# Kernel tuning notes

Hardware: AMD Instinct MI355X
Metric: run time of the kernel (lower is better)

The kernel has to match this reference:

```python
import jax, jax.numpy as jnp
import numpy as np

N, IN_DIM, OUT_DIM = 50000, 256, 64
K, DELTA_D = 8, 8            # k = out_dim // (ndim // init_k) = 64 // (64 // 8)
M = 1638400                  # edges
ROUTIT, TAU = 4, 1.0
EPS = 1e-12                  # F.normalize eps


def _l2norm(v, n, k, dd):
    # F.normalize over last dim of (n, k, dd) view, flattened back to (n, k*dd)
    v = v.reshape(n, k, dd)
    nrm = jnp.sqrt(jnp.sum(v * v, axis=2, keepdims=True))
    v = v / jnp.maximum(nrm, EPS)
    return v.reshape(n, k * dd)


def setup_inputs() -> dict:
    key = jax.random.key(0)
    k1, k2, k3, k4 = jax.random.split(key, 4)
    x = jax.random.normal(k1, (N, IN_DIM), dtype=jnp.float32)
    src_trg = jax.random.randint(k2, (2, M), 0, N, dtype=jnp.int64)
    std = 1.0 / np.sqrt(OUT_DIM)
    weight = jax.random.uniform(k3, (IN_DIM, OUT_DIM), dtype=jnp.float32, minval=-std, maxval=std)
    bias = jax.random.uniform(k4, (OUT_DIM,), dtype=jnp.float32, minval=-std, maxval=std)
    return {"x": x, "src_trg": src_trg, "weight": weight, "bias": bias}


def reference(x, src_trg, weight, bias):
    trg, src = src_trg[0], src_trg[1]
    n = x.shape[0]
    d = K * DELTA_D
    # DimReduceLayer + leaky_relu + per-capsule L2 normalize
    h = jax.nn.leaky_relu(x @ weight + bias)          # (n, d)
    h = _l2norm(h, n, K, DELTA_D)
    # RoutingLayer normalizes again (idempotent up to eps, kept for fidelity)
    h = _l2norm(h, n, K, DELTA_D)
    z = h[src].reshape(M, K, DELTA_D)                  # gather source capsules
    c = h
    for _ in range(ROUTIT):
        ct = c[trg].reshape(M, K, DELTA_D)             # gather target capsules
        p = jnp.sum(z * ct, axis=2)                    # (m, k) per-edge capsule scores
        p = jax.nn.softmax(p / TAU, axis=1)
        ws = (p[:, :, None] * z).reshape(M, d)         # weighted messages
        c = c.at[trg].add(ws)                          # scatter-add into targets
        c = _l2norm(c, n, K, DELTA_D)
    return c
```

## Files before the change

kernel.cpp:

```cpp
#include <hip/hip_runtime.h>
#include <math.h>
#include <stdint.h>

#define IN_DIM 256
#define OUT_D 64
#define ROUTIT 4
#define LCAP 48
#define NG 6
#define BSH 7
#define NBMAX 512
#define PEDGES 8192
#define LCCAP 6144

typedef float v2f __attribute__((ext_vector_type(2)));
__device__ __forceinline__ v2f pk_fma(v2f a, v2f b, v2f c) {
    return __builtin_elementwise_fma(a, b, c);
}

__device__ __forceinline__ float dpp_add_xor1(float x) {
    return x + __int_as_float(__builtin_amdgcn_mov_dpp(__float_as_int(x), 0xB1, 0xF, 0xF, true));
}
__device__ __forceinline__ float dpp_add_xor2(float x) {
    return x + __int_as_float(__builtin_amdgcn_mov_dpp(__float_as_int(x), 0x4E, 0xF, 0xF, true));
}
__device__ __forceinline__ float dpp_add_xor8(float x) {
    return x + __int_as_float(__builtin_amdgcn_mov_dpp(__float_as_int(x), 0x128, 0xF, 0xF, true));
}
__device__ __forceinline__ float swz_add_xor4(float x) {
    return x + __int_as_float(__builtin_amdgcn_ds_swizzle(__float_as_int(x), 0x101F));
}
__device__ __forceinline__ float swz_add_xor16(float x) {
    return x + __int_as_float(__builtin_amdgcn_ds_swizzle(__float_as_int(x), 0x401F));
}

__device__ __forceinline__ void load8p(v2f z[4], const float* p) {
    float4 a = *(const float4*)p;
    float4 b = *(const float4*)(p + 4);
    z[0] = (v2f){a.x, a.y}; z[1] = (v2f){a.z, a.w};
    z[2] = (v2f){b.x, b.y}; z[3] = (v2f){b.z, b.w};
}

__global__ __launch_bounds__(512, 2) void gemm_norm_kernel(
    const float* __restrict__ x, const float* __restrict__ w,
    const float* __restrict__ bias, float* __restrict__ h, int n)
{
    __shared__ float wlds[IN_DIM * OUT_D];
    {
        const float4* wsrc = (const float4*)w;
        float4* wdst = (float4*)wlds;
        #pragma unroll
        for (int i = 0; i < (IN_DIM * OUT_D / 4); i += 512)
            wdst[i + threadIdx.x] = wsrc[i + threadIdx.x];
    }
    __syncthreads();

    int lane = threadIdx.x & 63;
    int wv   = threadIdx.x >> 6;
    int c0   = wv * 8;
    int base = blockIdx.x * 256;

    const float* xr[4];
    int rows[4];
    #pragma unroll
    for (int r = 0; r < 4; ++r) {
        rows[r] = base + r * 64 + lane;
        int rc = rows[r] < n ? rows[r] : n - 1;
        xr[r] = x + (size_t)rc * IN_DIM;
    }

    v2f b2[4];
    #pragma unroll
    for (int j = 0; j < 4; ++j) b2[j] = (v2f){bias[c0 + 2*j], bias[c0 + 2*j + 1]};
    v2f acc[4][4];
    #pragma unroll
    for (int r = 0; r < 4; ++r)
        #pragma unroll
        for (int j = 0; j < 4; ++j) acc[r][j] = b2[j];

    float4 xa[4], xb[4];
    #pragma unroll
    for (int r = 0; r < 4; ++r) {
        xa[r] = *(const float4*)(xr[r]);
        xb[r] = *(const float4*)(xr[r] + 4);
    }

    for (int k0 = 0; k0 < IN_DIM; k0 += 8) {
        int kn = (k0 + 8 < IN_DIM) ? k0 + 8 : 0;
        float4 na[4], nb[4];
        #pragma unroll
        for (int r = 0; r < 4; ++r) {
            na[r] = *(const float4*)(xr[r] + kn);
            nb[r] = *(const float4*)(xr[r] + kn + 4);
        }
        const float* wk = wlds + k0 * OUT_D + c0;
        #pragma unroll
        for (int kk = 0; kk < 8; ++kk) {
            float4 w0 = *(const float4*)(wk + kk * OUT_D);
            float4 w1 = *(const float4*)(wk + kk * OUT_D + 4);
            v2f wvp[4] = {{w0.x,w0.y},{w0.z,w0.w},{w1.x,w1.y},{w1.z,w1.w}};
            #pragma unroll
            for (int r = 0; r < 4; ++r) {
                float xs = (kk < 4)
                    ? ((kk == 0) ? xa[r].x : (kk == 1) ? xa[r].y : (kk == 2) ? xa[r].z : xa[r].w)
                    : ((kk == 4) ? xb[r].x : (kk == 5) ? xb[r].y : (kk == 6) ? xb[r].z : xb[r].w);
                v2f xs2 = (v2f){xs, xs};
                acc[r][0] = pk_fma(xs2, wvp[0], acc[r][0]);
                acc[r][1] = pk_fma(xs2, wvp[1], acc[r][1]);
                acc[r][2] = pk_fma(xs2, wvp[2], acc[r][2]);
                acc[r][3] = pk_fma(xs2, wvp[3], acc[r][3]);
            }
        }
        #pragma unroll
        for (int r = 0; r < 4; ++r) { xa[r] = na[r]; xb[r] = nb[r]; }
    }

    #pragma unroll
    for (int r = 0; r < 4; ++r) {
        if (rows[r] < n) {
            float a[8];
            #pragma unroll
            for (int j = 0; j < 4; ++j) { a[2*j] = acc[r][j][0]; a[2*j+1] = acc[r][j][1]; }
            #pragma unroll
            for (int c = 0; c < 8; ++c) a[c] = a[c] > 0.0f ? a[c] : 0.01f * a[c];
            #pragma unroll
            for (int rep = 0; rep < 2; ++rep) {
                float ss = 0.0f;
                #pragma unroll
                for (int d = 0; d < 8; ++d) ss = fmaf(a[d], a[d], ss);
                float inv = 1.0f / fmaxf(sqrtf(ss), 1e-12f);
                #pragma unroll
                for (int d = 0; d < 8; ++d) a[d] *= inv;
            }
            float* hr = h + (size_t)rows[r] * OUT_D + c0;
            float4 o1, o2;
            o1.x=a[0]; o1.y=a[1]; o1.z=a[2]; o1.w=a[3];
            o2.x=a[4]; o2.y=a[5]; o2.z=a[6]; o2.w=a[7];
            *(float4*)hr = o1;
            *(float4*)(hr + 4) = o2;
        }
    }
}


__global__ __launch_bounds__(256) void bucket_hist_kernel(
    const int* __restrict__ trg, int m4, int* __restrict__ bucket_counts, int nb)
{
    __shared__ int hist[NBMAX];
    for (int i = threadIdx.x; i < nb; i += 256) hist[i] = 0;
    __syncthreads();
    for (int i = blockIdx.x * 256 + threadIdx.x; i < m4; i += 256 * gridDim.x) {
        int4 t = ((const int4*)trg)[i];
        atomicAdd(&hist[t.x >> BSH], 1);
        atomicAdd(&hist[t.y >> BSH], 1);
        atomicAdd(&hist[t.z >> BSH], 1);
        atomicAdd(&hist[t.w >> BSH], 1);
    }
    __syncthreads();
    for (int i = threadIdx.x; i < nb; i += 256) {
        int c = hist[i];
        if (c) atomicAdd(&bucket_counts[i], c);
    }
}

__global__ __launch_bounds__(64) void bucket_scan_kernel(
    const int* __restrict__ bucket_counts, int* __restrict__ bucket_base,
    int* __restrict__ bucket_cursor, int nb, int n, int m, int* __restrict__ row_start)
{
    int lane = threadIdx.x;
    int carry = 0;
    for (int base = 0; base <= nb; base += 64) {
        int i = base + lane;
        int v = (i < nb) ? bucket_counts[i] : 0;
        int s = v;
        #pragma unroll
        for (int off = 1; off < 64; off <<= 1) {
            int t = __shfl_up(s, off, 64);
            if (lane >= off) s += t;
        }
        if (i <= nb) {
            int exc = carry + s - v;
            bucket_base[i]   = exc;
            bucket_cursor[i] = exc;
        }
        carry += __shfl(s, 63, 64);
    }
    if (lane == 0) row_start[n] = m;
}

__global__ __launch_bounds__(1024) void partition_kernel(
    const int* __restrict__ trg, const int* __restrict__ src, int m4,
    uint32_t* __restrict__ epack, int* __restrict__ bucket_cursor, int nb)
{
    __shared__ uint32_t stage[PEDGES];
    __shared__ int hist[NBMAX];
    __shared__ int lbase[NBMAX];
    __shared__ int gdelta[NBMAX];
    for (int i = threadIdx.x; i < nb; i += 1024) hist[i] = 0;
    __syncthreads();
    int base4 = blockIdx.x * (PEDGES / 4);
    #pragma unroll
    for (int j = 0; j < PEDGES / 4 / 1024; ++j) {
        int i4 = base4 + j * 1024 + threadIdx.x;
        if (i4 < m4) {
            int4 t = ((const int4*)trg)[i4];
            atomicAdd(&hist[t.x >> BSH], 1);
            atomicAdd(&hist[t.y >> BSH], 1);
            atomicAdd(&hist[t.z >> BSH], 1);
            atomicAdd(&hist[t.w >> BSH], 1);
        }
    }
    __syncthreads();
    if (threadIdx.x < 64) {
        int lane = threadIdx.x;
        int carry = 0;
        for (int b0 = 0; b0 < nb; b0 += 64) {
            int i = b0 + lane;
            int v = (i < nb) ? hist[i] : 0;
            int s = v;
            #pragma unroll
            for (int off = 1; off < 64; off <<= 1) {
                int t = __shfl_up(s, off, 64);
                if (lane >= off) s += t;
            }
            if (i < nb) lbase[i] = carry + s - v;
            carry += __shfl(s, 63, 64);
        }
    }
    __syncthreads();
    for (int i = threadIdx.x; i < nb; i += 1024) {
        int c = hist[i];
        int g = c ? atomicAdd(&bucket_cursor[i], c) : 0;
        gdelta[i] = g - lbase[i];
    }
    __syncthreads();
    for (int i = threadIdx.x; i < nb; i += 1024) hist[i] = 0;
    __syncthreads();
    #pragma unroll
    for (int j = 0; j < PEDGES / 4 / 1024; ++j) {
        int i4 = base4 + j * 1024 + threadIdx.x;
        if (i4 < m4) {
            int4 t = ((const int4*)trg)[i4];
            int4 s = ((const int4*)src)[i4];
            int tt[4] = {t.x, t.y, t.z, t.w};
            int ss[4] = {s.x, s.y, s.z, s.w};
            #pragma unroll
            for (int q = 0; q < 4; ++q) {
                int b = tt[q] >> BSH;
                int r = atomicAdd(&hist[b], 1);
                stage[lbase[b] + r] = ((uint32_t)tt[q] << 16) | (uint32_t)ss[q];
            }
        }
    }
    __syncthreads();
    int rem = (m4 - base4) * 4;
    int cnt = rem < PEDGES ? rem : PEDGES;
    for (int i = threadIdx.x; i < cnt; i += 1024) {
        uint32_t p = stage[i];
        int b = (int)(p >> (16 + BSH));
        epack[gdelta[b] + i] = p;
    }
}

__global__ __launch_bounds__(512) void local_csr_kernel(
    const uint32_t* __restrict__ epack, const int* __restrict__ bucket_base,
    int* __restrict__ row_start, int* __restrict__ edge_src, int n)
{
    __shared__ int sorted[LCCAP];
    __shared__ int hist[128];
    __shared__ int excl[129];
    __shared__ int cursor[128];
    int b = blockIdx.x;
    int ebeg = bucket_base[b], eend = bucket_base[b + 1];
    int cnt = eend - ebeg;
    int node0 = b << BSH;
    if (threadIdx.x < 128) hist[threadIdx.x] = 0;
    __syncthreads();
    for (int e = threadIdx.x; e < cnt; e += 512)
        atomicAdd(&hist[(epack[ebeg + e] >> 16) & 127], 1);
    __syncthreads();
    if (threadIdx.x < 64) {
        int lane = threadIdx.x;
        int carry = 0;
        #pragma unroll
        for (int c = 0; c < 2; ++c) {
            int i = c * 64 + lane;
            int v = hist[i];
            int s = v;
            #pragma unroll
            for (int off = 1; off < 64; off <<= 1) {
                int t = __shfl_up(s, off, 64);
                if (lane >= off) s += t;
            }
            excl[i] = carry + s - v;
            carry += __shfl(s, 63, 64);
        }
        if (lane == 0) excl[128] = carry;
    }
    __syncthreads();
    int nh = n - node0; if (nh > 128) nh = 128;
    for (int i = threadIdx.x; i <= nh; i += 512)
        row_start[node0 + i] = ebeg + excl[i];
    if (threadIdx.x < 128) cursor[threadIdx.x] = excl[threadIdx.x];
    __syncthreads();
    for (int e = threadIdx.x; e < cnt; e += 512) {
        uint32_t p = epack[ebeg + e];
        int r = atomicAdd(&cursor[(p >> 16) & 127], 1);
        int sv = (int)(p & 0xFFFFu);
        if (r < LCCAP) sorted[r] = sv;
        else edge_src[ebeg + r] = sv;
    }
    __syncthreads();
    int lim = cnt < LCCAP ? cnt : LCCAP;
    for (int i = threadIdx.x; i < lim; i += 512)
        edge_src[ebeg + i] = sorted[i];
}

__device__ __forceinline__ void route_group(const v2f z[4], const v2f c[4], v2f acc[4]) {
    v2f p2 = z[0] * c[0];
    p2 = pk_fma(z[1], c[1], p2);
    p2 = pk_fma(z[2], c[2], p2);
    p2 = pk_fma(z[3], c[3], p2);
    float p = p2[0] + p2[1];
    float ex = __expf(p);
    float sm = dpp_add_xor1(ex);
    sm = dpp_add_xor2(sm);
    sm = dpp_add_xor8(sm);
    float wgt = __fdividef(ex, sm);
    v2f w2 = (v2f){wgt, wgt};
    acc[0] = pk_fma(w2, z[0], acc[0]);
    acc[1] = pk_fma(w2, z[1], acc[1]);
    acc[2] = pk_fma(w2, z[2], acc[2]);
    acc[3] = pk_fma(w2, z[3], acc[3]);
}

__global__ __launch_bounds__(256, 4) void route_kernel(
    const float* __restrict__ h, const int* __restrict__ row_start,
    const int* __restrict__ edge_src, float* __restrict__ out, int n)
{
    int lane = threadIdx.x & 63;
    int wid  = threadIdx.x >> 6;
    int v = blockIdx.x * 4 + wid;
    if (v >= n) return;
    int beg = row_start[v];
    int deg = row_start[v + 1] - beg;
    int nl  = deg < LCAP ? deg : LCAP;
    int ngroups = (nl + 7) >> 3;

    int k  = (lane & 3) | ((lane >> 1) & 4);
    int eo = ((lane >> 2) & 1) | ((lane >> 3) & 6);

    v2f c[4];
    load8p(c, h + (size_t)v * OUT_D + k * 8);

    v2f z[NG][4];
    #pragma unroll
    for (int g = 0; g < NG; ++g) {
        int e = g * 8 + eo;
        if (e < nl) {
            int s = edge_src[beg + e];
            load8p(z[g], h + (size_t)s * OUT_D + k * 8);
        } else {
            #pragma unroll
            for (int d = 0; d < 4; ++d) z[g][d] = (v2f){0.0f, 0.0f};
        }
    }

    #pragma unroll
    for (int it = 0; it < ROUTIT; ++it) {
        v2f acc[4] = {{0,0},{0,0},{0,0},{0,0}};
        #pragma unroll
        for (int g = 0; g < NG; ++g)
            if (g < ngroups) route_group(z[g], c, acc);
        if (deg > LCAP) {
            for (int e0 = LCAP; e0 < deg; e0 += 8) {
                int e = e0 + eo;
                v2f zt[4] = {{0,0},{0,0},{0,0},{0,0}};
                if (e < deg) {
                    int s = edge_src[beg + e];
                    load8p(zt, h + (size_t)s * OUT_D + k * 8);
                }
                route_group(zt, c, acc);
            }
        }
        float ss = 0.0f;
        #pragma unroll
        for (int d = 0; d < 8; ++d) {
            float a = acc[d >> 1][d & 1];
            a = swz_add_xor4(a);
            a = swz_add_xor16(a);
            a += __shfl_xor(a, 32, 64);
            float cv = c[d >> 1][d & 1] + a;
            c[d >> 1][d & 1] = cv;
            ss = fmaf(cv, cv, ss);
        }
        float inv = 1.0f / fmaxf(sqrtf(ss), 1e-12f);
        v2f inv2 = (v2f){inv, inv};
        #pragma unroll
        for (int j = 0; j < 4; ++j) c[j] *= inv2;
    }
    if (eo == 0) {
        float* op = out + (size_t)v * OUT_D + k * 8;
        float4 o1, o2;
        o1.x=c[0][0]; o1.y=c[0][1]; o1.z=c[1][0]; o1.w=c[1][1];
        o2.x=c[2][0]; o2.y=c[2][1]; o2.z=c[3][0]; o2.w=c[3][1];
        *(float4*)op = o1;
        *(float4*)(op + 4) = o2;
    }
}

extern "C" void kernel_launch(void* const* d_in, const int* in_sizes, int n_in,
                              void* d_out, int out_size, void* d_ws, size_t ws_size,
                              hipStream_t stream)
{
    const float* x       = (const float*)d_in[0];
    const int*   src_trg = (const int*)d_in[1];
    const float* w       = (const float*)d_in[2];
    const float* bias    = (const float*)d_in[3];
    float*       out     = (float*)d_out;

    int n = in_sizes[0] / IN_DIM;
    int m = in_sizes[1] / 2;
    int m4 = m >> 2;
    int nb = (n + 127) >> BSH;
    const int* trg = src_trg;
    const int* src = src_trg + m;

    char* wsb = (char*)d_ws;
    size_t off = 0;
    float*    h        = (float*)(wsb + off);    off += (size_t)n * OUT_D * sizeof(float);
    int*      rowstart = (int*)(wsb + off);      off += (size_t)(n + 1) * sizeof(int);
    off = (off + 255) & ~(size_t)255;
    int*      edgesrc  = (int*)(wsb + off);      off += (size_t)m * sizeof(int);
    off = (off + 255) & ~(size_t)255;
    uint32_t* epack    = (uint32_t*)(wsb + off); off += (size_t)m * sizeof(uint32_t);
    int*      bcounts  = (int*)(wsb + off);      off += (size_t)(nb + 1) * sizeof(int);
    int*      bbase    = (int*)(wsb + off);      off += (size_t)(nb + 1) * sizeof(int);
    int*      bcursor  = (int*)(wsb + off);      off += (size_t)(nb + 1) * sizeof(int);

    hipMemsetAsync(bcounts, 0, (size_t)(nb + 1) * sizeof(int), stream);
    gemm_norm_kernel<<<(n + 255) / 256, 512, 0, stream>>>(x, w, bias, h, n);
    bucket_hist_kernel<<<256, 256, 0, stream>>>(trg, m4, bcounts, nb);
    bucket_scan_kernel<<<1, 64, 0, stream>>>(bcounts, bbase, bcursor, nb, n, m, rowstart);
    partition_kernel<<<(m + PEDGES - 1) / PEDGES, 1024, 0, stream>>>(trg, src, m4, epack, bcursor, nb);
    local_csr_kernel<<<nb, 512, 0, stream>>>(epack, bbase, rowstart, edgesrc, n);
    route_kernel<<<(n + 3) / 4, 256, 0, stream>>>(h, rowstart, edgesrc, out, n);
}
```

Baseline: 273.2 us.

## Fuse bucket histogram into GEMM launch, halve bucket size, pad global counters

```diff
diff --git a/kernel.cpp b/kernel.cpp
--- a/kernel.cpp
+++ b/kernel.cpp
@@ -7,10 +7,11 @@
 #define ROUTIT 4
 #define LCAP 48
 #define NG 6
-#define BSH 7
-#define NBMAX 512
-#define PEDGES 8192
-#define LCCAP 6144
+#define BSH 6
+#define NBMAX 800
+#define PEDGES 4096
+#define LCCAP 3072
+#define HISTB 128
 
 typedef float v2f __attribute__((ext_vector_type(2)));
 __device__ __forceinline__ v2f pk_fma(v2f a, v2f b, v2f c) {
@@ -40,11 +41,32 @@
     z[2] = (v2f){b.x, b.y}; z[3] = (v2f){b.z, b.w};
 }
 
-__global__ __launch_bounds__(512, 2) void gemm_norm_kernel(
+__global__ __launch_bounds__(512, 2) void gemm_hist_kernel(
     const float* __restrict__ x, const float* __restrict__ w,
-    const float* __restrict__ bias, float* __restrict__ h, int n)
+    const float* __restrict__ bias, float* __restrict__ h, int n,
+    const int* __restrict__ trg, int m4, int* __restrict__ bpad, int nb)
 {
     __shared__ float wlds[IN_DIM * OUT_D];
+
+    if (blockIdx.x < HISTB) {
+        int* hist = (int*)wlds;
+        for (int i = threadIdx.x; i < nb; i += 512) hist[i] = 0;
+        __syncthreads();
+        for (int i = blockIdx.x * 512 + threadIdx.x; i < m4; i += 512 * HISTB) {
+            int4 t = ((const int4*)trg)[i];
+            atomicAdd(&hist[t.x >> BSH], 1);
+            atomicAdd(&hist[t.y >> BSH], 1);
+            atomicAdd(&hist[t.z >> BSH], 1);
+            atomicAdd(&hist[t.w >> BSH], 1);
+        }
+        __syncthreads();
+        for (int i = threadIdx.x; i < nb; i += 512) {
+            int c = hist[i];
+            if (c) atomicAdd(&bpad[i << 4], c);
+        }
+        return;
+    }
+
     {
         const float4* wsrc = (const float4*)w;
         float4* wdst = (float4*)wlds;
@@ -57,7 +79,7 @@
     int lane = threadIdx.x & 63;
     int wv   = threadIdx.x >> 6;
     int c0   = wv * 8;
-    int base = blockIdx.x * 256;
+    int base = (blockIdx.x - HISTB) * 256;
 
     const float* xr[4];
     int rows[4];
@@ -86,11 +108,11 @@
 
     for (int k0 = 0; k0 < IN_DIM; k0 += 8) {
         int kn = (k0 + 8 < IN_DIM) ? k0 + 8 : 0;
-        float4 na[4], nb[4];
+        float4 na[4], nb4[4];
         #pragma unroll
         for (int r = 0; r < 4; ++r) {
-            na[r] = *(const float4*)(xr[r] + kn);
-            nb[r] = *(const float4*)(xr[r] + kn + 4);
+            na[r]  = *(const float4*)(xr[r] + kn);
+            nb4[r] = *(const float4*)(xr[r] + kn + 4);
         }
         const float* wk = wlds + k0 * OUT_D + c0;
         #pragma unroll
@@ -111,7 +133,7 @@
             }
         }
         #pragma unroll
-        for (int r = 0; r < 4; ++r) { xa[r] = na[r]; xb[r] = nb[r]; }
+        for (int r = 0; r < 4; ++r) { xa[r] = na[r]; xb[r] = nb4[r]; }
     }
 
     #pragma unroll
@@ -141,55 +163,34 @@
     }
 }
 
-
-__global__ __launch_bounds__(256) void bucket_hist_kernel(
-    const int* __restrict__ trg, int m4, int* __restrict__ bucket_counts, int nb)
-{
-    __shared__ int hist[NBMAX];
-    for (int i = threadIdx.x; i < nb; i += 256) hist[i] = 0;
-    __syncthreads();
-    for (int i = blockIdx.x * 256 + threadIdx.x; i < m4; i += 256 * gridDim.x) {
-        int4 t = ((const int4*)trg)[i];
-        atomicAdd(&hist[t.x >> BSH], 1);
-        atomicAdd(&hist[t.y >> BSH], 1);
-        atomicAdd(&hist[t.z >> BSH], 1);
-        atomicAdd(&hist[t.w >> BSH], 1);
-    }
-    __syncthreads();
-    for (int i = threadIdx.x; i < nb; i += 256) {
-        int c = hist[i];
-        if (c) atomicAdd(&bucket_counts[i], c);
-    }
-}
-
 __global__ __launch_bounds__(64) void bucket_scan_kernel(
-    const int* __restrict__ bucket_counts, int* __restrict__ bucket_base,
-    int* __restrict__ bucket_cursor, int nb, int n, int m, int* __restrict__ row_start)
+    int* __restrict__ bpad, int* __restrict__ bucket_base,
+    int nb, int n, int m, int* __restrict__ row_start)
 {
     int lane = threadIdx.x;
     int carry = 0;
-    for (int base = 0; base <= nb; base += 64) {
+    for (int base = 0; base < nb; base += 64) {
         int i = base + lane;
-        int v = (i < nb) ? bucket_counts[i] : 0;
+        int v = (i < nb) ? bpad[i << 4] : 0;
         int s = v;
         #pragma unroll
         for (int off = 1; off < 64; off <<= 1) {
             int t = __shfl_up(s, off, 64);
             if (lane >= off) s += t;
         }
-        if (i <= nb) {
+        if (i < nb) {
             int exc = carry + s - v;
-            bucket_base[i]   = exc;
-            bucket_cursor[i] = exc;
+            bucket_base[i] = exc;
+            bpad[i << 4]   = exc;
         }
         carry += __shfl(s, 63, 64);
     }
-    if (lane == 0) row_start[n] = m;
+    if (lane == 0) { bucket_base[nb] = m; row_start[n] = m; }
 }
 
 __global__ __launch_bounds__(1024) void partition_kernel(
     const int* __restrict__ trg, const int* __restrict__ src, int m4,
-    uint32_t* __restrict__ epack, int* __restrict__ bucket_cursor, int nb)
+    uint32_t* __restrict__ epack, int* __restrict__ bpad, int nb)
 {
     __shared__ uint32_t stage[PEDGES];
     __shared__ int hist[NBMAX];
@@ -197,17 +198,16 @@
     __shared__ int gdelta[NBMAX];
     for (int i = threadIdx.x; i < nb; i += 1024) hist[i] = 0;
     __syncthreads();
-    int base4 = blockIdx.x * (PEDGES / 4);
-    #pragma unroll
-    for (int j = 0; j < PEDGES / 4 / 1024; ++j) {
-        int i4 = base4 + j * 1024 + threadIdx.x;
-        if (i4 < m4) {
-            int4 t = ((const int4*)trg)[i4];
-            atomicAdd(&hist[t.x >> BSH], 1);
-            atomicAdd(&hist[t.y >> BSH], 1);
-            atomicAdd(&hist[t.z >> BSH], 1);
-            atomicAdd(&hist[t.w >> BSH], 1);
-        }
+    int i4 = blockIdx.x * (PEDGES / 4) + threadIdx.x;
+    int4 t = make_int4(-1,-1,-1,-1), s = make_int4(0,0,0,0);
+    bool valid = i4 < m4;
+    if (valid) {
+        t = ((const int4*)trg)[i4];
+        s = ((const int4*)src)[i4];
+        atomicAdd(&hist[t.x >> BSH], 1);
+        atomicAdd(&hist[t.y >> BSH], 1);
+        atomicAdd(&hist[t.z >> BSH], 1);
+        atomicAdd(&hist[t.w >> BSH], 1);
     }
     __syncthreads();
     if (threadIdx.x < 64) {
@@ -216,43 +216,37 @@
         for (int b0 = 0; b0 < nb; b0 += 64) {
             int i = b0 + lane;
             int v = (i < nb) ? hist[i] : 0;
-            int s = v;
+            int sc = v;
             #pragma unroll
             for (int off = 1; off < 64; off <<= 1) {
-                int t = __shfl_up(s, off, 64);
-                if (lane >= off) s += t;
+                int u = __shfl_up(sc, off, 64);
+                if (lane >= off) sc += u;
             }
-            if (i < nb) lbase[i] = carry + s - v;
-            carry += __shfl(s, 63, 64);
+            if (i < nb) lbase[i] = carry + sc - v;
+            carry += __shfl(sc, 63, 64);
         }
     }
     __syncthreads();
     for (int i = threadIdx.x; i < nb; i += 1024) {
         int c = hist[i];
-        int g = c ? atomicAdd(&bucket_cursor[i], c) : 0;
+        int g = c ? atomicAdd(&bpad[i << 4], c) : 0;
         gdelta[i] = g - lbase[i];
     }
     __syncthreads();
     for (int i = threadIdx.x; i < nb; i += 1024) hist[i] = 0;
     __syncthreads();
-    #pragma unroll
-    for (int j = 0; j < PEDGES / 4 / 1024; ++j) {
-        int i4 = base4 + j * 1024 + threadIdx.x;
-        if (i4 < m4) {
-            int4 t = ((const int4*)trg)[i4];
-            int4 s = ((const int4*)src)[i4];
-            int tt[4] = {t.x, t.y, t.z, t.w};
-            int ss[4] = {s.x, s.y, s.z, s.w};
-            #pragma unroll
-            for (int q = 0; q < 4; ++q) {
-                int b = tt[q] >> BSH;
-                int r = atomicAdd(&hist[b], 1);
-                stage[lbase[b] + r] = ((uint32_t)tt[q] << 16) | (uint32_t)ss[q];
-            }
-        }
-    }
-    __syncthreads();
-    int rem = (m4 - base4) * 4;
+    if (valid) {
+        int tt[4] = {t.x, t.y, t.z, t.w};
+        int ss[4] = {s.x, s.y, s.z, s.w};
+        #pragma unroll
+        for (int q = 0; q < 4; ++q) {
+            int b = tt[q] >> BSH;
+            int r = atomicAdd(&hist[b], 1);
+            stage[lbase[b] + r] = ((uint32_t)tt[q] << 16) | (uint32_t)ss[q];
+        }
+    }
+    __syncthreads();
+    int rem = (m4 - blockIdx.x * (PEDGES / 4)) * 4;
     int cnt = rem < PEDGES ? rem : PEDGES;
     for (int i = threadIdx.x; i < cnt; i += 1024) {
         uint32_t p = stage[i];
@@ -266,45 +260,39 @@
     int* __restrict__ row_start, int* __restrict__ edge_src, int n)
 {
     __shared__ int sorted[LCCAP];
-    __shared__ int hist[128];
-    __shared__ int excl[129];
-    __shared__ int cursor[128];
+    __shared__ int hist[64];
+    __shared__ int excl[65];
+    __shared__ int cursor[64];
     int b = blockIdx.x;
     int ebeg = bucket_base[b], eend = bucket_base[b + 1];
     int cnt = eend - ebeg;
     int node0 = b << BSH;
-    if (threadIdx.x < 128) hist[threadIdx.x] = 0;
+    if (threadIdx.x < 64) hist[threadIdx.x] = 0;
     __syncthreads();
     for (int e = threadIdx.x; e < cnt; e += 512)
-        atomicAdd(&hist[(epack[ebeg + e] >> 16) & 127], 1);
+        atomicAdd(&hist[(epack[ebeg + e] >> 16) & 63], 1);
     __syncthreads();
     if (threadIdx.x < 64) {
         int lane = threadIdx.x;
-        int carry = 0;
-        #pragma unroll
-        for (int c = 0; c < 2; ++c) {
-            int i = c * 64 + lane;
-            int v = hist[i];
-            int s = v;
-            #pragma unroll
-            for (int off = 1; off < 64; off <<= 1) {
-                int t = __shfl_up(s, off, 64);
-                if (lane >= off) s += t;
-            }
-            excl[i] = carry + s - v;
-            carry += __shfl(s, 63, 64);
-        }
-        if (lane == 0) excl[128] = carry;
-    }
-    __syncthreads();
-    int nh = n - node0; if (nh > 128) nh = 128;
+        int v = hist[lane];
+        int s = v;
+        #pragma unroll
+        for (int off = 1; off < 64; off <<= 1) {
+            int u = __shfl_up(s, off, 64);
+            if (lane >= off) s += u;
+        }
+        excl[lane] = s - v;
+        if (lane == 63) excl[64] = s;
+    }
+    __syncthreads();
+    int nh = n - node0; if (nh > 64) nh = 64;
     for (int i = threadIdx.x; i <= nh; i += 512)
         row_start[node0 + i] = ebeg + excl[i];
-    if (threadIdx.x < 128) cursor[threadIdx.x] = excl[threadIdx.x];
+    if (threadIdx.x < 64) cursor[threadIdx.x] = excl[threadIdx.x];
     __syncthreads();
     for (int e = threadIdx.x; e < cnt; e += 512) {
         uint32_t p = epack[ebeg + e];
-        int r = atomicAdd(&cursor[(p >> 16) & 127], 1);
+        int r = atomicAdd(&cursor[(p >> 16) & 63], 1);
         int sv = (int)(p & 0xFFFFu);
         if (r < LCCAP) sorted[r] = sv;
         else edge_src[ebeg + r] = sv;
@@ -421,7 +409,7 @@
     int n = in_sizes[0] / IN_DIM;
     int m = in_sizes[1] / 2;
     int m4 = m >> 2;
-    int nb = (n + 127) >> BSH;
+    int nb = (n + 63) >> BSH;
     const int* trg = src_trg;
     const int* src = src_trg + m;
 
@@ -433,15 +421,15 @@
     int*      edgesrc  = (int*)(wsb + off);      off += (size_t)m * sizeof(int);
     off = (off + 255) & ~(size_t)255;
     uint32_t* epack    = (uint32_t*)(wsb + off); off += (size_t)m * sizeof(uint32_t);
-    int*      bcounts  = (int*)(wsb + off);      off += (size_t)(nb + 1) * sizeof(int);
     int*      bbase    = (int*)(wsb + off);      off += (size_t)(nb + 1) * sizeof(int);
-    int*      bcursor  = (int*)(wsb + off);      off += (size_t)(nb + 1) * sizeof(int);
-
-    hipMemsetAsync(bcounts, 0, (size_t)(nb + 1) * sizeof(int), stream);
-    gemm_norm_kernel<<<(n + 255) / 256, 512, 0, stream>>>(x, w, bias, h, n);
-    bucket_hist_kernel<<<256, 256, 0, stream>>>(trg, m4, bcounts, nb);
-    bucket_scan_kernel<<<1, 64, 0, stream>>>(bcounts, bbase, bcursor, nb, n, m, rowstart);
-    partition_kernel<<<(m + PEDGES - 1) / PEDGES, 1024, 0, stream>>>(trg, src, m4, epack, bcursor, nb);
+    off = (off + 255) & ~(size_t)255;
+    int*      bpad     = (int*)(wsb + off);      off += (size_t)nb * 16 * sizeof(int);
+
+    int gemmb = (n + 255) / 256;
+    hipMemsetAsync(bpad, 0, (size_t)nb * 16 * sizeof(int), stream);
+    gemm_hist_kernel<<<HISTB + gemmb, 512, 0, stream>>>(x, w, bias, h, n, trg, m4, bpad, nb);
+    bucket_scan_kernel<<<1, 64, 0, stream>>>(bpad, bbase, nb, n, m, rowstart);
+    partition_kernel<<<(m + PEDGES - 1) / PEDGES, 1024, 0, stream>>>(trg, src, m4, epack, bpad, nb);
     local_csr_kernel<<<nb, 512, 0, stream>>>(epack, bbase, rowstart, edgesrc, n);
     route_kernel<<<(n + 3) / 4, 256, 0, stream>>>(h, rowstart, edgesrc, out, n);
 }
```

New measurement: 275.5 us. Within noise of the previous version (+0.8%).
